# Performance work log

Hardware: AMD Instinct MI355X
Metric: run time of the kernel (lower is better)

The kernel has to match this reference:

```python
import jax, jax.numpy as jnp
import numpy as np

# scNET (vae_flag=False, cd=False, eval mode): genes x cells matrix;
# PPI graph over 3000 genes, KNN graph over 4096 cells.
N_GENES, N_CELLS = 3000, 4096          # col_dim, row_dim
INTER_R, EMBD_R = 512, 128             # gene (rows) encoder dims
INTER_C, EMBD_C = 1024, 256            # cell (cols) encoder dims
N_LAYERS = 2
KNN_E, PPI_E = 65536, 262144
SCALE_PARAM = 3.0                      # TransformerConvReducrLayer scale_param


def setup_inputs() -> dict:
    key = jax.random.key(0)
    ks = iter(jax.random.split(key, 64))
    def lin(shape):
        fan_in = shape[-2]
        return jax.random.normal(next(ks), shape, jnp.float32) / np.sqrt(fan_in)
    inp = {}
    inp["x"] = jax.random.normal(next(ks), (N_GENES, N_CELLS), jnp.float32)
    inp["knn_ei"] = jax.random.randint(next(ks), (2, KNN_E), 0, N_CELLS)
    inp["ppi_ei"] = jax.random.randint(next(ks), (2, PPI_E), 0, N_GENES)
    inp["rl_W"] = lin((N_CELLS, N_CELLS)); inp["rl_b"] = jnp.zeros((N_CELLS,), jnp.float32)
    inp["rs_Wl"] = lin((N_LAYERS, N_CELLS, N_CELLS)); inp["rs_Wr"] = lin((N_LAYERS, N_CELLS, N_CELLS))
    inp["rs_b"] = jnp.zeros((N_LAYERS, N_CELLS), jnp.float32)
    inp["cs_Wl"] = lin((N_LAYERS, N_GENES, N_GENES)); inp["cs_Wr"] = lin((N_LAYERS, N_GENES, N_GENES))
    inp["cs_b"] = jnp.zeros((N_LAYERS, N_GENES), jnp.float32)
    inp["rg_W"] = lin((N_CELLS, INTER_R)); inp["rg_b"] = jnp.zeros((INTER_R,), jnp.float32)
    for nm in ("rq", "rk", "rv", "rsk"):
        inp[nm + "_W"] = lin((INTER_R, EMBD_R)); inp[nm + "_b"] = jnp.zeros((EMBD_R,), jnp.float32)
    inp["cg_W"] = lin((N_GENES, INTER_C)); inp["cg_b"] = jnp.zeros((INTER_C,), jnp.float32)
    for nm in ("cq", "ck", "cv", "csk"):
        inp[nm + "_W"] = lin((INTER_C, EMBD_C)); inp[nm + "_b"] = jnp.zeros((EMBD_C,), jnp.float32)
    inp["d1_W"] = lin((EMBD_C, INTER_C)); inp["d1_b"] = jnp.zeros((INTER_C,), jnp.float32)
    inp["d2_W"] = lin((INTER_C, INTER_C)); inp["d2_b"] = jnp.zeros((INTER_C,), jnp.float32)
    inp["d3_W"] = lin((INTER_C, N_GENES)); inp["d3_b"] = jnp.zeros((N_GENES,), jnp.float32)
    return inp


def sage_conv(x, ei, Wl, Wr, b):
    # PyG SAGEConv (mean aggr, root weight): lin_l(mean_{j->i} x_j) + lin_r(x_i) + b
    n = x.shape[0]
    src, dst = ei[0], ei[1]
    s = jax.ops.segment_sum(x[src], dst, num_segments=n)
    cnt = jax.ops.segment_sum(jnp.ones((ei.shape[1],), x.dtype), dst, num_segments=n)
    agg = s / jnp.maximum(cnt, 1.0)[:, None]
    return agg @ Wl + x @ Wr + b


def gcn_conv(x, ei, W, b):
    # PyG GCNConv: self loops + symmetric D^-1/2 (A+I) D^-1/2 normalization
    n = x.shape[0]
    idx = jnp.arange(n)
    src = jnp.concatenate([ei[0], idx])
    dst = jnp.concatenate([ei[1], idx])
    deg = jax.ops.segment_sum(jnp.ones((src.shape[0],), x.dtype), dst, num_segments=n)
    dinv = jax.lax.rsqrt(jnp.maximum(deg, 1.0))
    h = x @ W
    msg = h[src] * (dinv[src] * dinv[dst])[:, None]
    return jax.ops.segment_sum(msg, dst, num_segments=n) + b


def transformer_conv(x, ei, Wq, bq, Wk, bk, Wv, bv, Ws, bs, scale_param):
    # PyG TransformerConv (heads=1). scale_param=None -> per-destination segment
    # softmax; otherwise scNET's globally sigmoid-normalized attention
    # (TransformerConvReducrLayer.message): global mean/std standardize -> sigmoid.
    n = x.shape[0]
    d = Wq.shape[1]
    src, dst = ei[0], ei[1]
    q = x @ Wq + bq
    k = x @ Wk + bk
    v = x @ Wv + bv
    alpha = (q[dst] * k[src]).sum(-1) / jnp.sqrt(jnp.asarray(d, x.dtype))  # [E]
    if scale_param is None:
        m = jax.ops.segment_max(alpha, dst, num_segments=n)
        e = jnp.exp(alpha - m[dst])
        z = jax.ops.segment_sum(e, dst, num_segments=n)
        alpha = e / (z[dst] + 1e-16)
    else:
        alpha = (alpha - alpha.mean()) / ((1.0 / scale_param) * jnp.std(alpha, ddof=1))
        alpha = jax.nn.sigmoid(alpha)
    out = jax.ops.segment_sum(v[src] * alpha[:, None], dst, num_segments=n)
    return out + (x @ Ws + bs)  # root skip (lin_skip)


def reference(x, knn_ei, ppi_ei, rl_W, rl_b, rs_Wl, rs_Wr, rs_b, cs_Wl, cs_Wr, cs_b,
              rg_W, rg_b, rq_W, rq_b, rk_W, rk_b, rv_W, rv_b, rsk_W, rsk_b,
              cg_W, cg_b, cq_W, cq_b, ck_W, ck_b, cv_W, cv_b, csk_W, csk_b,
              d1_W, d1_b, d2_W, d2_b, d3_W, d3_b):
    # MutaelEncoder: row linear then alternating col/row SAGE layers (dropout=id in eval)
    h = x @ rl_W + rl_b                                   # [G, C]
    for i in range(N_LAYERS):
        h = jax.nn.leaky_relu(sage_conv(h.T, knn_ei, cs_Wl[i], cs_Wr[i], cs_b[i]), 0.01).T
        h = jax.nn.leaky_relu(sage_conv(h, ppi_ei, rs_Wl[i], rs_Wr[i], rs_b[i]), 0.01)
    # rows (gene) DimEncoder: GCN -> LeakyReLU -> TransformerConv (softmax attention)
    r = jax.nn.leaky_relu(gcn_conv(h, ppi_ei, rg_W, rg_b), 0.01)
    row_embed = transformer_conv(r, ppi_ei, rq_W, rq_b, rk_W, rk_b, rv_W, rv_b, rsk_W, rsk_b, None)
    # cols (cell) DimEncoder (reducer): GCN -> LeakyReLU -> sigmoid-normalized attention
    c = jax.nn.leaky_relu(gcn_conv(h.T, knn_ei, cg_W, cg_b), 0.01)
    col_embed = transformer_conv(c, knn_ei, cq_W, cq_b, ck_W, ck_b, cv_W, cv_b, csk_W, csk_b, SCALE_PARAM)
    # FatureDecoder (cd=False): 3-layer MLP with ReLU (dropout=id in eval)
    d = jax.nn.relu(col_embed @ d1_W + d1_b)
    d = jax.nn.relu(d @ d2_W + d2_b)
    recon = d @ d3_W + d3_b                               # [C_cells, G]
    return row_embed, col_embed, recon
```

## Files before the change

kernel.cpp:

```cpp
#include <hip/hip_runtime.h>
#include <math.h>

#define N_GENES 3000
#define N_CELLS 4096
#define GPAD    3072
#define INTER_R 512
#define EMBD_R  128
#define INTER_C 1024
#define EMBD_C  256
#define KNN_E   65536
#define PPI_E   262144

typedef unsigned short u16;
typedef __bf16 bf16x8 __attribute__((ext_vector_type(8)));
typedef float f32x4 __attribute__((ext_vector_type(4)));

__device__ __forceinline__ float b2f(u16 u) {
  union { unsigned i; float f; } x; x.i = ((unsigned)u) << 16; return x.f;
}
__device__ __forceinline__ u16 f2b(float f) {
  union { float f; unsigned i; } x; x.f = f;
  unsigned r = (x.i + 0x7FFFu + ((x.i >> 16) & 1u)) >> 16;
  return (u16)r;
}

typedef const void __attribute__((address_space(1))) gvoid;
typedef void __attribute__((address_space(3))) svoid;
__device__ __forceinline__ void gload16(const void* g, void* l) {
  __builtin_amdgcn_global_load_lds((gvoid*)g, (svoid*)l, 16, 0, 0);
}

template <int OUTF32>
__global__ __launch_bounds__(256) void mgemm_k(
    const u16* __restrict__ A, int lda, const u16* __restrict__ BT, int ldb,
    const float* __restrict__ bias, void* __restrict__ Cv, int ldc,
    int M, int N, int K, int accum, int act, int nbx) {
  __shared__ u16 As[2][64 * 64];
  __shared__ u16 Bs[2][64 * 64];
  const int t = threadIdx.x;
  const int w = t >> 6, l = t & 63;
  const int wr = w >> 1, wc = w & 1;
  const int fr = l & 15, hi = l >> 4;

  int nwg = gridDim.x, bid = blockIdx.x;
  int q = nwg >> 3, r = nwg & 7, xcd = bid & 7, seq = bid >> 3;
  int sid = (xcd < r ? xcd * (q + 1) : r * (q + 1) + (xcd - r) * q) + seq;
  int by = sid / nbx, bx = sid - by * nbx;
  const int row0 = by * 128, col0 = bx * 128;

  f32x4 acc[4][4];
#pragma unroll
  for (int i = 0; i < 4; i++)
#pragma unroll
    for (int j = 0; j < 4; j++) acc[i][j] = (f32x4){0.f, 0.f, 0.f, 0.f};

  const u16* Aad[2]; const u16* Bad[2];
  char* Alds[2]; char* Blds[2];
#pragma unroll
  for (int c = 0; c < 2; c++) {
    int P = (w * 2 + c) * 64 + l;
    int prow = P >> 3, s = P & 7;
    int lr = prow * 2 + (s >> 2);
    int g = (s & 3) ^ (prow & 3);
    int ar = row0 + lr; ar = ar < M ? ar : M - 1;
    int br = col0 + lr; br = br < N ? br : N - 1;
    Aad[c] = A + (size_t)ar * lda + g * 8;
    Bad[c] = BT + (size_t)br * ldb + g * 8;
    Alds[c] = (char*)&As[0][0] + P * 16;
    Blds[c] = (char*)&Bs[0][0] + P * 16;
  }
  const int nt = K >> 5;
  auto stage = [&](int tt, int b) {
    int ko = tt << 5;
#pragma unroll
    for (int c = 0; c < 2; c++) {
      gload16(Aad[c] + ko, Alds[c] + b * 8192);
      gload16(Bad[c] + ko, Blds[c] + b * 8192);
    }
  };
  auto compute = [&](int tt) {
    const u16* Ab = As[tt & 1];
    const u16* Bb = Bs[tt & 1];
    bf16x8 af[4], bfr[4];
#pragma unroll
    for (int mi = 0; mi < 4; mi++) {
      int row = wr * 64 + mi * 16 + fr;
      int pr = row >> 1;
      af[mi] = *(const bf16x8*)&Ab[pr * 64 + ((row & 1) * 4 + (hi ^ (pr & 3))) * 8];
    }
#pragma unroll
    for (int ni = 0; ni < 4; ni++) {
      int row = wc * 64 + ni * 16 + fr;
      int pr = row >> 1;
      bfr[ni] = *(const bf16x8*)&Bb[pr * 64 + ((row & 1) * 4 + (hi ^ (pr & 3))) * 8];
    }
    __builtin_amdgcn_s_setprio(1);
#pragma unroll
    for (int mi = 0; mi < 4; mi++)
#pragma unroll
      for (int ni = 0; ni < 4; ni++)
        acc[mi][ni] = __builtin_amdgcn_mfma_f32_16x16x32_bf16(
            af[mi], bfr[ni], acc[mi][ni], 0, 0, 0);
    __builtin_amdgcn_s_setprio(0);
  };

  stage(0, 0);
  if (nt > 1) stage(1, 1);
  for (int tt = 0; tt < nt - 1; tt++) {
    asm volatile("s_waitcnt vmcnt(4)" ::: "memory");
    __builtin_amdgcn_sched_barrier(0);
    __builtin_amdgcn_s_barrier();
    __builtin_amdgcn_sched_barrier(0);
    compute(tt);
    __builtin_amdgcn_sched_barrier(0);
    __builtin_amdgcn_s_barrier();
    __builtin_amdgcn_sched_barrier(0);
    if (tt + 2 < nt) stage(tt + 2, tt & 1);
  }
  asm volatile("s_waitcnt vmcnt(0)" ::: "memory");
  __builtin_amdgcn_sched_barrier(0);
  __builtin_amdgcn_s_barrier();
  __builtin_amdgcn_sched_barrier(0);
  compute(nt - 1);

#pragma unroll
  for (int mi = 0; mi < 4; mi++) {
    int mb = row0 + wr * 64 + mi * 16 + hi * 4;
#pragma unroll
    for (int rr2 = 0; rr2 < 4; rr2++) {
      int m = mb + rr2;
      if (m >= M) continue;
#pragma unroll
      for (int ni = 0; ni < 4; ni++) {
        int n = col0 + wc * 64 + ni * 16 + fr;
        if (n >= N) continue;
        float v = acc[mi][ni][rr2];
        if (bias) v += bias[n];
        if (OUTF32) {
          float* C = (float*)Cv;
          if (accum) v += C[(size_t)m * ldc + n];
          if (act == 1) v = v > 0.f ? v : 0.01f * v;
          else if (act == 2) v = fmaxf(v, 0.f);
          C[(size_t)m * ldc + n] = v;
        } else {
          u16* C = (u16*)Cv;
          if (accum) v += b2f(C[(size_t)m * ldc + n]);
          if (act == 1) v = v > 0.f ? v : 0.01f * v;
          else if (act == 2) v = fmaxf(v, 0.f);
          C[(size_t)m * ldc + n] = f2b(v);
        }
      }
    }
  }
}

__global__ void cvtw_k(const float* __restrict__ in, int K, int Nw,
                       u16* __restrict__ out, int ldb, int Kpad) {
  __shared__ float tile[32][33];
  int k0 = blockIdx.y * 32, n0 = blockIdx.x * 32;
  int tx = threadIdx.x & 31, ty = threadIdx.x >> 5;
  for (int i = ty; i < 32; i += 8)
    tile[i][tx] = (k0 + i < K && n0 + tx < Nw) ? in[(size_t)(k0 + i) * Nw + n0 + tx] : 0.f;
  __syncthreads();
  for (int i = ty; i < 32; i += 8) {
    int n = n0 + i, k = k0 + tx;
    if (n < Nw && k < Kpad) out[(size_t)n * ldb + k] = f2b(tile[tx][i]);
  }
}

__global__ void tpad_k(const u16* __restrict__ in, int R, int C, int lin,
                       u16* __restrict__ out, int ostride, int Rpad) {
  __shared__ u16 tile[32][33];
  int r0 = blockIdx.y * 32, c0 = blockIdx.x * 32;
  int tx = threadIdx.x & 31, ty = threadIdx.x >> 5;
  for (int i = ty; i < 32; i += 8)
    tile[i][tx] = (r0 + i < R && c0 + tx < C) ? in[(size_t)(r0 + i) * lin + c0 + tx] : (u16)0;
  __syncthreads();
  for (int i = ty; i < 32; i += 8) {
    int c = c0 + i, r = r0 + tx;
    if (c < C && r < Rpad) out[(size_t)c * ostride + r] = tile[tx][i];
  }
}

__global__ void cvtx_k(const float* __restrict__ in, u16* __restrict__ out, int n) {
  int i = (blockIdx.x * 256 + threadIdx.x) * 4;
  if (i >= n) return;
  float4 v = *(const float4*)&in[i];
  uint2 o;
  o.x = (unsigned)f2b(v.x) | ((unsigned)f2b(v.y) << 16);
  o.y = (unsigned)f2b(v.z) | ((unsigned)f2b(v.w) << 16);
  *(uint2*)&out[i] = o;
}

__global__ void catbias_k(const float* b0, const float* b1, const float* b2,
                          const float* b3, int seg, float* out) {
  int i = blockIdx.x * 256 + threadIdx.x;
  if (i >= 4 * seg) return;
  const float* s = i < seg ? b0 : i < 2 * seg ? b1 : i < 3 * seg ? b2 : b3;
  out[i] = s[i & (seg - 1)];
}

__global__ void zero_i32(int* __restrict__ p, int n) {
  int i = blockIdx.x * 256 + threadIdx.x;
  if (i < n) p[i] = 0;
}
__global__ void count_k(const int* __restrict__ dst, int E, int* __restrict__ cnt) {
  int e = blockIdx.x * 256 + threadIdx.x;
  if (e < E) atomicAdd(&cnt[dst[e]], 1);
}
__global__ __launch_bounds__(1024) void scan_k(const int* __restrict__ cnt,
                                               int* __restrict__ rs, int N) {
  __shared__ int sd[1024];
  int t = threadIdx.x;
  int per = (N + 1023) >> 10;
  int base = t * per;
  int loc[4];
  int s = 0;
  for (int u = 0; u < per; u++) {
    int idx = base + u;
    loc[u] = s;
    int v = (idx < N) ? cnt[idx] : 0;
    s += v;
  }
  sd[t] = s;
  __syncthreads();
  for (int off = 1; off < 1024; off <<= 1) {
    int v = (t >= off) ? sd[t - off] : 0;
    __syncthreads();
    sd[t] += v;
    __syncthreads();
  }
  int prev = (t > 0) ? sd[t - 1] : 0;
  for (int u = 0; u < per; u++) {
    int idx = base + u;
    if (idx < N) rs[idx] = prev + loc[u];
  }
  if (t == 0) rs[N] = sd[1023];
}
__global__ void fill_k(const int* __restrict__ src, const int* __restrict__ dst, int E,
                       const int* __restrict__ rs, int* cursor,
                       int* __restrict__ csrc, int* __restrict__ ceid) {
  int e = blockIdx.x * 256 + threadIdx.x;
  if (e >= E) return;
  int d = dst[e];
  int p = atomicAdd(&cursor[d], 1);
  int b = rs[d] + p;
  csrc[b] = src[e];
  ceid[b] = e;
}
__global__ void dinv_k(const int* __restrict__ rs, float* __restrict__ dinv, int N) {
  int i = blockIdx.x * 256 + threadIdx.x;
  if (i < N) dinv[i] = rsqrtf((float)(rs[i + 1] - rs[i] + 1));
}

__global__ void sage_agg_k(const u16* __restrict__ X, int ld, const int* __restrict__ rs,
                           const int* __restrict__ csrc, u16* __restrict__ out, int D) {
  int i = blockIdx.y;
  int j8 = (blockIdx.x * 256 + threadIdx.x) * 8;
  if (j8 >= D) return;
  int s = rs[i], e = rs[i + 1];
  float a[8] = {0, 0, 0, 0, 0, 0, 0, 0};
  for (int p = s; p < e; p++) {
    uint4 v = *(const uint4*)&X[(size_t)csrc[p] * ld + j8];
    a[0] += b2f(v.x & 0xffff); a[1] += b2f(v.x >> 16);
    a[2] += b2f(v.y & 0xffff); a[3] += b2f(v.y >> 16);
    a[4] += b2f(v.z & 0xffff); a[5] += b2f(v.z >> 16);
    a[6] += b2f(v.w & 0xffff); a[7] += b2f(v.w >> 16);
  }
  float inv = 1.f / fmaxf((float)(e - s), 1.f);
  uint4 o;
  o.x = (unsigned)f2b(a[0] * inv) | ((unsigned)f2b(a[1] * inv) << 16);
  o.y = (unsigned)f2b(a[2] * inv) | ((unsigned)f2b(a[3] * inv) << 16);
  o.z = (unsigned)f2b(a[4] * inv) | ((unsigned)f2b(a[5] * inv) << 16);
  o.w = (unsigned)f2b(a[6] * inv) | ((unsigned)f2b(a[7] * inv) << 16);
  *(uint4*)&out[(size_t)i * ld + j8] = o;
}

__global__ void gcn_agg_k(const u16* __restrict__ HW, int ld, const int* __restrict__ rs,
                          const int* __restrict__ csrc, const float* __restrict__ dinv,
                          const float* __restrict__ bias, u16* __restrict__ out, int D) {
  int i = blockIdx.y;
  int j8 = (blockIdx.x * 256 + threadIdx.x) * 8;
  if (j8 >= D) return;
  int s = rs[i], e = rs[i + 1];
  float a[8] = {0, 0, 0, 0, 0, 0, 0, 0};
  for (int p = s; p < e; p++) {
    int sr = csrc[p];
    float w = dinv[sr];
    uint4 v = *(const uint4*)&HW[(size_t)sr * ld + j8];
    a[0] += b2f(v.x & 0xffff) * w; a[1] += b2f(v.x >> 16) * w;
    a[2] += b2f(v.y & 0xffff) * w; a[3] += b2f(v.y >> 16) * w;
    a[4] += b2f(v.z & 0xffff) * w; a[5] += b2f(v.z >> 16) * w;
    a[6] += b2f(v.w & 0xffff) * w; a[7] += b2f(v.w >> 16) * w;
  }
  float di = dinv[i];
  uint4 sv = *(const uint4*)&HW[(size_t)i * ld + j8];
  float sf[8] = {b2f(sv.x & 0xffff), b2f(sv.x >> 16), b2f(sv.y & 0xffff), b2f(sv.y >> 16),
                 b2f(sv.z & 0xffff), b2f(sv.z >> 16), b2f(sv.w & 0xffff), b2f(sv.w >> 16)};
  unsigned o[4];
#pragma unroll
  for (int q = 0; q < 4; q++) {
    float v0 = di * a[2 * q] + sf[2 * q] * di * di + bias[j8 + 2 * q];
    float v1 = di * a[2 * q + 1] + sf[2 * q + 1] * di * di + bias[j8 + 2 * q + 1];
    v0 = v0 > 0.f ? v0 : 0.01f * v0;
    v1 = v1 > 0.f ? v1 : 0.01f * v1;
    o[q] = (unsigned)f2b(v0) | ((unsigned)f2b(v1) << 16);
  }
  *(uint4*)&out[(size_t)i * ld + j8] = *(uint4*)o;
}

__global__ void attn_row_k(const u16* __restrict__ QKVS, const int* __restrict__ rs,
                           const int* __restrict__ csrc, float* __restrict__ out, int N) {
  int node = blockIdx.x * 4 + (threadIdx.x >> 6);
  if (node >= N) return;
  int lane = threadIdx.x & 63;
  const u16* base = QKVS + (size_t)node * 512;
  unsigned qb = *(const unsigned*)&base[lane * 2];
  float qx = b2f(qb & 0xffff), qy = b2f(qb >> 16);
  int s = rs[node], e = rs[node + 1];
  float m = -1e30f, z = 0.f, ax = 0.f, ay = 0.f;
  const float scale = 0.08838834764831845f;
  for (int p = s; p < e; p++) {
    const u16* kb = QKVS + (size_t)csrc[p] * 512;
    unsigned kw = *(const unsigned*)&kb[128 + lane * 2];
    float part = qx * b2f(kw & 0xffff) + qy * b2f(kw >> 16);
#pragma unroll
    for (int off = 32; off; off >>= 1) part += __shfl_xor(part, off);
    float a = part * scale;
    float mn = fmaxf(m, a);
    float sc = __expf(m - mn);
    float wv = __expf(a - mn);
    z = z * sc + wv;
    unsigned vw = *(const unsigned*)&kb[256 + lane * 2];
    ax = ax * sc + wv * b2f(vw & 0xffff);
    ay = ay * sc + wv * b2f(vw >> 16);
    m = mn;
  }
  float inv = (e == s) ? 0.f : 1.f / (z + 1e-16f);
  unsigned sw = *(const unsigned*)&base[384 + lane * 2];
  out[(size_t)node * 128 + lane * 2] = ax * inv + b2f(sw & 0xffff);
  out[(size_t)node * 128 + lane * 2 + 1] = ay * inv + b2f(sw >> 16);
}

__global__ void col_alpha_k(const u16* __restrict__ QKVS, const int* __restrict__ src,
                            const int* __restrict__ dst, float* __restrict__ alpha, int E) {
  int e = blockIdx.x * 4 + (threadIdx.x >> 6);
  if (e >= E) return;
  int lane = threadIdx.x & 63;
  uint2 qb = *(const uint2*)&QKVS[(size_t)dst[e] * 1024 + lane * 4];
  uint2 kb = *(const uint2*)&QKVS[(size_t)src[e] * 1024 + 256 + lane * 4];
  float p = b2f(qb.x & 0xffff) * b2f(kb.x & 0xffff) + b2f(qb.x >> 16) * b2f(kb.x >> 16) +
            b2f(qb.y & 0xffff) * b2f(kb.y & 0xffff) + b2f(qb.y >> 16) * b2f(kb.y >> 16);
#pragma unroll
  for (int off = 32; off; off >>= 1) p += __shfl_xor(p, off);
  if (lane == 0) alpha[e] = p * 0.0625f;
}

__global__ void stats_k(const float* __restrict__ alpha, int E, double* __restrict__ st) {
  __shared__ double s1[256], s2[256];
  int t = threadIdx.x;
  double a1 = 0, a2 = 0;
  for (int i = blockIdx.x * 256 + t; i < E; i += gridDim.x * 256) {
    double a = alpha[i];
    a1 += a; a2 += a * a;
  }
  s1[t] = a1; s2[t] = a2;
  __syncthreads();
  for (int off = 128; off; off >>= 1) {
    if (t < off) { s1[t] += s1[t + off]; s2[t] += s2[t + off]; }
    __syncthreads();
  }
  if (t == 0) { atomicAdd(&st[0], s1[0]); atomicAdd(&st[1], s2[0]); }
}

__global__ void col_attn_agg_k(const u16* __restrict__ QKVS, const float* __restrict__ alpha,
                               const int* __restrict__ rs, const int* __restrict__ csrc,
                               const int* __restrict__ ceid, const double* __restrict__ st,
                               float* __restrict__ outf, u16* __restrict__ outb, int E) {
  int i = blockIdx.x;
  int j = threadIdx.x;
  double mean = st[0] / E;
  double var = (st[1] - E * mean * mean) / (double)(E - 1);
  float rstd = (float)(1.0 / sqrt(var));
  float fm = (float)mean;
  int s = rs[i], e = rs[i + 1];
  float acc = 0.f;
  for (int p = s; p < e; p++) {
    float a = alpha[ceid[p]];
    float x = 3.0f * (a - fm) * rstd;
    float sg = 1.f / (1.f + __expf(-x));
    acc += sg * b2f(QKVS[(size_t)csrc[p] * 1024 + 512 + j]);
  }
  float res = acc + b2f(QKVS[(size_t)i * 1024 + 768 + j]);
  outf[(size_t)i * 256 + j] = res;
  outb[(size_t)i * 256 + j] = f2b(res);
}

extern "C" void kernel_launch(void* const* d_in, const int* in_sizes, int n_in,
                              void* d_out, int out_size, void* d_ws, size_t ws_size,
                              hipStream_t stream) {
  const float* x      = (const float*)d_in[0];
  const int*   knn_ei = (const int*)d_in[1];
  const int*   ppi_ei = (const int*)d_in[2];
  const float* rl_W   = (const float*)d_in[3];
  const float* rl_b   = (const float*)d_in[4];
  const float* rs_Wl  = (const float*)d_in[5];
  const float* rs_Wr  = (const float*)d_in[6];
  const float* rs_b   = (const float*)d_in[7];
  const float* cs_Wl  = (const float*)d_in[8];
  const float* cs_Wr  = (const float*)d_in[9];
  const float* cs_b   = (const float*)d_in[10];
  const float* rg_W   = (const float*)d_in[11];
  const float* rg_b   = (const float*)d_in[12];
  const float* rq_W   = (const float*)d_in[13];
  const float* rq_b   = (const float*)d_in[14];
  const float* rk_W   = (const float*)d_in[15];
  const float* rk_b   = (const float*)d_in[16];
  const float* rv_W   = (const float*)d_in[17];
  const float* rv_b   = (const float*)d_in[18];
  const float* rsk_W  = (const float*)d_in[19];
  const float* rsk_b  = (const float*)d_in[20];
  const float* cg_W   = (const float*)d_in[21];
  const float* cg_b   = (const float*)d_in[22];
  const float* cq_W   = (const float*)d_in[23];
  const float* cq_b   = (const float*)d_in[24];
  const float* ck_W   = (const float*)d_in[25];
  const float* ck_b   = (const float*)d_in[26];
  const float* cv_W   = (const float*)d_in[27];
  const float* cv_b   = (const float*)d_in[28];
  const float* csk_W  = (const float*)d_in[29];
  const float* csk_b  = (const float*)d_in[30];
  const float* d1_W   = (const float*)d_in[31];
  const float* d1_b   = (const float*)d_in[32];
  const float* d2_W   = (const float*)d_in[33];
  const float* d2_b   = (const float*)d_in[34];
  const float* d3_W   = (const float*)d_in[35];
  const float* d3_b   = (const float*)d_in[36];
  float* out = (float*)d_out;

  char* ws = (char*)d_ws;
  size_t off = 0;
  auto alloc = [&](size_t bytes) -> void* {
    void* p = ws + off;
    off = (off + bytes + 255) & ~(size_t)255;
    return p;
  };
  u16* P0 = (u16*)alloc((size_t)N_GENES * N_CELLS * 2);
  u16* P1 = (u16*)alloc((size_t)N_CELLS * GPAD * 2);
  u16* P2 = (u16*)alloc((size_t)N_CELLS * GPAD * 2);
  u16* CR = (u16*)alloc((size_t)N_CELLS * 2 * GPAD * 2);
  u16* BTs = (u16*)alloc((size_t)N_CELLS * 2 * N_CELLS * 2);
  u16* CEb = (u16*)alloc((size_t)N_CELLS * EMBD_C * 2);
  float* catb = (float*)alloc(1024 * 4);
  int* knn_rs  = (int*)alloc((N_CELLS + 1) * 4);
  int* knn_cnt = (int*)alloc(N_CELLS * 4);
  int* knn_cur = (int*)alloc(N_CELLS * 4);
  int* knn_src = (int*)alloc(KNN_E * 4);
  int* knn_eid = (int*)alloc(KNN_E * 4);
  int* ppi_rs  = (int*)alloc((N_GENES + 1) * 4);
  int* ppi_cnt = (int*)alloc(N_GENES * 4);
  int* ppi_cur = (int*)alloc(N_GENES * 4);
  int* ppi_src = (int*)alloc(PPI_E * 4);
  int* ppi_eid = (int*)alloc(PPI_E * 4);
  float* dinv_knn = (float*)alloc(N_CELLS * 4);
  float* dinv_ppi = (float*)alloc(N_GENES * 4);
  float* alphaB   = (float*)alloc(KNN_E * 4);
  double* stats   = (double*)alloc(2 * 8);
  u16* xb = CR;
  u16* CA = CR;
  u16* RA = CR;

  auto cvtw = [&](const float* W, int K, int Nw, u16* dst, int ldb, int Kpad) {
    dim3 g((Nw + 31) / 32, (Kpad + 31) / 32);
    cvtw_k<<<g, 256, 0, stream>>>(W, K, Nw, dst, ldb, Kpad);
  };
  auto mg = [&](const u16* A, int lda, const u16* BT, int ldb, const float* bias,
                void* C, int ldc, int M, int N, int K, int accum, int act, int outf32) {
    int nbx = (N + 127) / 128, nby = (M + 127) / 128;
    dim3 g(nbx * nby);
    if (outf32)
      mgemm_k<1><<<g, 256, 0, stream>>>(A, lda, BT, ldb, bias, C, ldc, M, N, K, accum, act, nbx);
    else
      mgemm_k<0><<<g, 256, 0, stream>>>(A, lda, BT, ldb, bias, C, ldc, M, N, K, accum, act, nbx);
  };
  auto tpad = [&](const u16* in, int R, int C, int lin, u16* o, int ostride, int Rpad) {
    dim3 g((C + 31) / 32, (Rpad + 31) / 32);
    tpad_k<<<g, 256, 0, stream>>>(in, R, C, lin, o, ostride, Rpad);
  };
  auto sage = [&](const u16* X, int ld, const int* rs, const int* csrc, u16* o,
                  int nodes, int D) {
    dim3 g((D / 8 + 255) / 256, nodes);
    sage_agg_k<<<g, 256, 0, stream>>>(X, ld, rs, csrc, o, D);
  };
  auto gcn = [&](const u16* HW, int ld, const int* rs, const int* csrc, const float* dinv,
                 const float* bias, u16* o, int nodes, int D) {
    dim3 g((D / 8 + 255) / 256, nodes);
    gcn_agg_k<<<g, 256, 0, stream>>>(HW, ld, rs, csrc, dinv, bias, o, D);
  };

  zero_i32<<<(N_CELLS + 255) / 256, 256, 0, stream>>>(knn_cnt, N_CELLS);
  count_k<<<(KNN_E + 255) / 256, 256, 0, stream>>>(knn_ei + KNN_E, KNN_E, knn_cnt);
  scan_k<<<1, 1024, 0, stream>>>(knn_cnt, knn_rs, N_CELLS);
  zero_i32<<<(N_CELLS + 255) / 256, 256, 0, stream>>>(knn_cur, N_CELLS);
  fill_k<<<(KNN_E + 255) / 256, 256, 0, stream>>>(knn_ei, knn_ei + KNN_E, KNN_E,
                                                  knn_rs, knn_cur, knn_src, knn_eid);
  dinv_k<<<(N_CELLS + 255) / 256, 256, 0, stream>>>(knn_rs, dinv_knn, N_CELLS);
  zero_i32<<<(N_GENES + 255) / 256, 256, 0, stream>>>(ppi_cnt, N_GENES);
  count_k<<<(PPI_E + 255) / 256, 256, 0, stream>>>(ppi_ei + PPI_E, PPI_E, ppi_cnt);
  scan_k<<<1, 1024, 0, stream>>>(ppi_cnt, ppi_rs, N_GENES);
  zero_i32<<<(N_GENES + 255) / 256, 256, 0, stream>>>(ppi_cur, N_GENES);
  fill_k<<<(PPI_E + 255) / 256, 256, 0, stream>>>(ppi_ei, ppi_ei + PPI_E, PPI_E,
                                                  ppi_rs, ppi_cur, ppi_src, ppi_eid);
  dinv_k<<<(N_GENES + 255) / 256, 256, 0, stream>>>(ppi_rs, dinv_ppi, N_GENES);

  cvtx_k<<<(N_GENES * N_CELLS / 4 + 255) / 256, 256, 0, stream>>>(
      x, xb, N_GENES * N_CELLS);
  cvtw(rl_W, N_CELLS, N_CELLS, BTs, N_CELLS, N_CELLS);
  mg(xb, N_CELLS, BTs, N_CELLS, rl_b, P0, N_CELLS, N_GENES, N_CELLS, N_CELLS, 0, 0, 0);

  for (int i = 0; i < 2; i++) {
    const float* cWl = cs_Wl + (size_t)i * N_GENES * N_GENES;
    const float* cWr = cs_Wr + (size_t)i * N_GENES * N_GENES;
    const float* cb  = cs_b + (size_t)i * N_GENES;
    const float* rWl = rs_Wl + (size_t)i * N_CELLS * N_CELLS;
    const float* rWr = rs_Wr + (size_t)i * N_CELLS * N_CELLS;
    const float* rb  = rs_b + (size_t)i * N_CELLS;
    tpad(P0, N_GENES, N_CELLS, N_CELLS, CA + GPAD, 2 * GPAD, GPAD);
    sage(CA + GPAD, 2 * GPAD, knn_rs, knn_src, CA, N_CELLS, GPAD);
    cvtw(cWl, N_GENES, N_GENES, BTs, 2 * GPAD, GPAD);
    cvtw(cWr, N_GENES, N_GENES, BTs + GPAD, 2 * GPAD, GPAD);
    mg(CA, 2 * GPAD, BTs, 2 * GPAD, cb, P1, GPAD, N_CELLS, N_GENES, 2 * GPAD, 0, 1, 0);
    tpad(P1, N_CELLS, N_GENES, GPAD, RA + N_CELLS, 2 * N_CELLS, N_CELLS);
    sage(RA + N_CELLS, 2 * N_CELLS, ppi_rs, ppi_src, RA, N_GENES, N_CELLS);
    cvtw(rWl, N_CELLS, N_CELLS, BTs, 2 * N_CELLS, N_CELLS);
    cvtw(rWr, N_CELLS, N_CELLS, BTs + N_CELLS, 2 * N_CELLS, N_CELLS);
    mg(RA, 2 * N_CELLS, BTs, 2 * N_CELLS, rb, P0, N_CELLS,
       N_GENES, N_CELLS, 2 * N_CELLS, 0, 1, 0);
  }

  cvtw(rg_W, N_CELLS, INTER_R, BTs, N_CELLS, N_CELLS);
  mg(P0, N_CELLS, BTs, N_CELLS, nullptr, P1, INTER_R, N_GENES, INTER_R, N_CELLS, 0, 0, 0);
  gcn(P1, INTER_R, ppi_rs, ppi_src, dinv_ppi, rg_b, P2, N_GENES, INTER_R);
  cvtw(rq_W, INTER_R, EMBD_R, BTs + (size_t)0 * EMBD_R * INTER_R, INTER_R, INTER_R);
  cvtw(rk_W, INTER_R, EMBD_R, BTs + (size_t)1 * EMBD_R * INTER_R, INTER_R, INTER_R);
  cvtw(rv_W, INTER_R, EMBD_R, BTs + (size_t)2 * EMBD_R * INTER_R, INTER_R, INTER_R);
  cvtw(rsk_W, INTER_R, EMBD_R, BTs + (size_t)3 * EMBD_R * INTER_R, INTER_R, INTER_R);
  catbias_k<<<2, 256, 0, stream>>>(rq_b, rk_b, rv_b, rsk_b, EMBD_R, catb);
  mg(P2, INTER_R, BTs, INTER_R, catb, P1, 4 * EMBD_R, N_GENES, 4 * EMBD_R, INTER_R, 0, 0, 0);
  attn_row_k<<<(N_GENES + 3) / 4, 256, 0, stream>>>(P1, ppi_rs, ppi_src, out, N_GENES);

  tpad(P0, N_GENES, N_CELLS, N_CELLS, P1, GPAD, GPAD);
  cvtw(cg_W, N_GENES, INTER_C, BTs, GPAD, GPAD);
  mg(P1, GPAD, BTs, GPAD, nullptr, P2, INTER_C, N_CELLS, INTER_C, GPAD, 0, 0, 0);
  gcn(P2, INTER_C, knn_rs, knn_src, dinv_knn, cg_b, P0, N_CELLS, INTER_C);
  cvtw(cq_W, INTER_C, EMBD_C, BTs + (size_t)0 * EMBD_C * INTER_C, INTER_C, INTER_C);
  cvtw(ck_W, INTER_C, EMBD_C, BTs + (size_t)1 * EMBD_C * INTER_C, INTER_C, INTER_C);
  cvtw(cv_W, INTER_C, EMBD_C, BTs + (size_t)2 * EMBD_C * INTER_C, INTER_C, INTER_C);
  cvtw(csk_W, INTER_C, EMBD_C, BTs + (size_t)3 * EMBD_C * INTER_C, INTER_C, INTER_C);
  catbias_k<<<4, 256, 0, stream>>>(cq_b, ck_b, cv_b, csk_b, EMBD_C, catb);
  mg(P0, INTER_C, BTs, INTER_C, catb, P1, 4 * EMBD_C, N_CELLS, 4 * EMBD_C, INTER_C, 0, 0, 0);
  col_alpha_k<<<KNN_E / 4, 256, 0, stream>>>(P1, knn_ei, knn_ei + KNN_E, alphaB, KNN_E);
  zero_i32<<<1, 256, 0, stream>>>((int*)stats, 4);
  stats_k<<<64, 256, 0, stream>>>(alphaB, KNN_E, stats);
  float* col_embed = out + (size_t)N_GENES * EMBD_R;
  col_attn_agg_k<<<N_CELLS, 256, 0, stream>>>(P1, alphaB, knn_rs, knn_src, knn_eid,
                                              stats, col_embed, CEb, KNN_E);

  u16* D1 = CR;
  u16* D2 = CR + (size_t)N_CELLS * INTER_C;
  float* recon = col_embed + (size_t)N_CELLS * EMBD_C;
  cvtw(d1_W, EMBD_C, INTER_C, BTs, EMBD_C, EMBD_C);
  mg(CEb, EMBD_C, BTs, EMBD_C, d1_b, D1, INTER_C, N_CELLS, INTER_C, EMBD_C, 0, 2, 0);
  cvtw(d2_W, INTER_C, INTER_C, BTs, INTER_C, INTER_C);
  mg(D1, INTER_C, BTs, INTER_C, d2_b, D2, INTER_C, N_CELLS, INTER_C, INTER_C, 0, 2, 0);
  cvtw(d3_W, INTER_C, N_GENES, BTs, INTER_C, INTER_C);
  mg(D2, INTER_C, BTs, INTER_C, d3_b, recon, N_GENES, N_CELLS, N_GENES, INTER_C, 0, 0, 1);
}
```

Baseline: 2.434 ms.

## Add 256x256 eight-wave pipelined GEMM and slab-wise SAGE aggregation

Adds a new bf16 MFMA GEMM kernel with 256x256 tiles, 512 threads, a swizzled LDS layout, global_load_lds staging and a hand-scheduled double-buffered pipeline. It replaces the old 128x128 GEMM for the large square matmuls and the final decoder layer. The larger tile is meant to raise data reuse per byte loaded and to overlap loads with MFMA work. SAGE aggregation becomes one wave per node, launched once per 512-column slab, which should improve gather locality. The large tiles leave fewer workgroups for the 3000-row problems, and the partial edge tiles waste compute.

New measurement: 2.648 ms. 1.09x slower.

```diff
diff --git a/kernel.cpp b/kernel.cpp
--- a/kernel.cpp
+++ b/kernel.cpp
@@ -28,6 +28,168 @@
 typedef void __attribute__((address_space(3))) svoid;
 __device__ __forceinline__ void gload16(const void* g, void* l) {
   __builtin_amdgcn_global_load_lds((gvoid*)g, (svoid*)l, 16, 0, 0);
+}
+
+template <int OUTF32>
+__global__ __launch_bounds__(512, 1) void mgemm8_k(
+    const u16* __restrict__ A, int lda, const u16* __restrict__ BT, int ldb,
+    const float* __restrict__ bias, void* __restrict__ Cv, int ldc,
+    int M, int N, int K, int accum, int act, int nbx) {
+  __shared__ u16 S[65536];
+  const int t = threadIdx.x;
+  const int wid = t >> 6, l = t & 63;
+  const int wm = wid >> 2, wn = wid & 3;
+  const int fr = l & 15, hi = l >> 4;
+
+  int nwg = gridDim.x, bid = blockIdx.x;
+  int q = nwg >> 3, r = nwg & 7, xcd = bid & 7, seq = bid >> 3;
+  int sid = (xcd < r ? xcd * (q + 1) : r * (q + 1) + (xcd - r) * q) + seq;
+  int by = sid / nbx, bx = sid - by * nbx;
+  const int row0 = by * 256, col0 = bx * 256;
+
+  f32x4 acc[8][4];
+#pragma unroll
+  for (int i = 0; i < 8; i++)
+#pragma unroll
+    for (int j = 0; j < 4; j++) acc[i][j] = (f32x4){0.f, 0.f, 0.f, 0.f};
+
+  int r1 = t >> 2, r2 = r1 + 128;
+  int g1 = (t & 3) ^ ((r1 >> 1) & 3);
+  int g2 = (t & 3) ^ ((r2 >> 1) & 3);
+  int ar1 = row0 + r1; ar1 = ar1 < M ? ar1 : M - 1;
+  int ar2 = row0 + r2; ar2 = ar2 < M ? ar2 : M - 1;
+  int br1 = col0 + r1; br1 = br1 < N ? br1 : N - 1;
+  int br2 = col0 + r2; br2 = br2 < N ? br2 : N - 1;
+  const u16* baseA1 = A + (size_t)ar1 * lda + g1 * 8;
+  const u16* baseA2 = A + (size_t)ar2 * lda + g2 * 8;
+  const u16* baseB1 = BT + (size_t)br1 * ldb + g1 * 8;
+  const u16* baseB2 = BT + (size_t)br2 * ldb + g2 * 8;
+
+  bf16x8 af[4], bfr[4];
+
+#define STAGEA(buf, kh, kt) { \
+  int ko_ = (kt) * 64 + (kh) * 32; \
+  gload16(baseA1 + ko_, (char*)&S[((buf) * 4 + (kh)) * 8192] + t * 16); \
+  gload16(baseA2 + ko_, (char*)&S[((buf) * 4 + (kh)) * 8192] + (t + 512) * 16); }
+#define STAGEB(buf, kh, kt) { \
+  int ko_ = (kt) * 64 + (kh) * 32; \
+  gload16(baseB1 + ko_, (char*)&S[((buf) * 4 + 2 + (kh)) * 8192] + t * 16); \
+  gload16(baseB2 + ko_, (char*)&S[((buf) * 4 + 2 + (kh)) * 8192] + (t + 512) * 16); }
+#define DSRA(buf, kh, mh) \
+  _Pragma("unroll") \
+  for (int i_ = 0; i_ < 4; i_++) { \
+    int row_ = wm * 128 + ((mh) * 4 + i_) * 16 + fr; \
+    af[i_] = *(const bf16x8*)&S[((buf) * 4 + (kh)) * 8192 + row_ * 32 + \
+                                ((hi ^ ((row_ >> 1) & 3)) << 3)]; \
+  }
+#define DSRB(buf, kh) \
+  _Pragma("unroll") \
+  for (int i_ = 0; i_ < 4; i_++) { \
+    int row_ = wn * 64 + i_ * 16 + fr; \
+    bfr[i_] = *(const bf16x8*)&S[((buf) * 4 + 2 + (kh)) * 8192 + row_ * 32 + \
+                                 ((hi ^ ((row_ >> 1) & 3)) << 3)]; \
+  }
+#define MMA(mh) \
+  __builtin_amdgcn_s_setprio(1); \
+  _Pragma("unroll") \
+  for (int i_ = 0; i_ < 4; i_++) { \
+    _Pragma("unroll") \
+    for (int j_ = 0; j_ < 4; j_++) \
+      acc[(mh) * 4 + i_][j_] = __builtin_amdgcn_mfma_f32_16x16x32_bf16( \
+          af[i_], bfr[j_], acc[(mh) * 4 + i_][j_], 0, 0, 0); \
+  } \
+  __builtin_amdgcn_s_setprio(0);
+#define BARMID \
+  __builtin_amdgcn_sched_barrier(0); \
+  __builtin_amdgcn_s_barrier(); \
+  asm volatile("s_waitcnt lgkmcnt(0)" ::: "memory"); \
+  __builtin_amdgcn_sched_barrier(0);
+#define BAREND \
+  __builtin_amdgcn_sched_barrier(0); \
+  __builtin_amdgcn_s_barrier(); \
+  __builtin_amdgcn_sched_barrier(0);
+
+  const int nt = K >> 6;
+  STAGEA(0, 0, 0); STAGEB(0, 0, 0); STAGEA(0, 1, 0); STAGEB(0, 1, 0);
+  STAGEA(1, 0, 1); STAGEB(1, 0, 1); STAGEA(1, 1, 1);
+  asm volatile("s_waitcnt vmcnt(6)" ::: "memory");
+  __builtin_amdgcn_sched_barrier(0);
+  __builtin_amdgcn_s_barrier();
+  __builtin_amdgcn_sched_barrier(0);
+
+  int p = 0;
+  for (int kt = 0; kt < nt - 2; kt++, p ^= 1) {
+    DSRA(p, 0, 0); DSRB(p, 0);
+    STAGEB(p ^ 1, 1, kt + 1);
+    BARMID; MMA(0); BAREND;
+    DSRA(p, 0, 1);
+    STAGEA(p, 0, kt + 2);
+    BARMID; MMA(1); BAREND;
+    DSRA(p, 1, 0); DSRB(p, 1);
+    STAGEB(p, 0, kt + 2);
+    BARMID; MMA(0); BAREND;
+    DSRA(p, 1, 1);
+    STAGEA(p, 1, kt + 2);
+    asm volatile("s_waitcnt vmcnt(6)" ::: "memory");
+    BARMID; MMA(1); BAREND;
+  }
+  DSRA(p, 0, 0); DSRB(p, 0);
+  STAGEB(p ^ 1, 1, nt - 1);
+  BARMID; MMA(0); BAREND;
+  DSRA(p, 0, 1);
+  BARMID; MMA(1); BAREND;
+  DSRA(p, 1, 0); DSRB(p, 1);
+  BARMID; MMA(0); BAREND;
+  DSRA(p, 1, 1);
+  asm volatile("s_waitcnt vmcnt(0)" ::: "memory");
+  BARMID; MMA(1); BAREND;
+  p ^= 1;
+  DSRA(p, 0, 0); DSRB(p, 0);
+  BARMID; MMA(0); BAREND;
+  DSRA(p, 0, 1);
+  BARMID; MMA(1); BAREND;
+  DSRA(p, 1, 0); DSRB(p, 1);
+  BARMID; MMA(0); BAREND;
+  DSRA(p, 1, 1);
+  BARMID; MMA(1); BAREND;
+
+#undef STAGEA
+#undef STAGEB
+#undef DSRA
+#undef DSRB
+#undef MMA
+#undef BARMID
+#undef BAREND
+
+#pragma unroll
+  for (int mf = 0; mf < 8; mf++) {
+    int mb = row0 + wm * 128 + mf * 16 + hi * 4;
+#pragma unroll
+    for (int rr2 = 0; rr2 < 4; rr2++) {
+      int m = mb + rr2;
+      if (m >= M) continue;
+#pragma unroll
+      for (int nf = 0; nf < 4; nf++) {
+        int n = col0 + wn * 64 + nf * 16 + fr;
+        if (n >= N) continue;
+        float v = acc[mf][nf][rr2];
+        if (bias) v += bias[n];
+        if (OUTF32) {
+          float* C = (float*)Cv;
+          if (accum) v += C[(size_t)m * ldc + n];
+          if (act == 1) v = v > 0.f ? v : 0.01f * v;
+          else if (act == 2) v = fmaxf(v, 0.f);
+          C[(size_t)m * ldc + n] = v;
+        } else {
+          u16* C = (u16*)Cv;
+          if (accum) v += b2f(C[(size_t)m * ldc + n]);
+          if (act == 1) v = v > 0.f ? v : 0.01f * v;
+          else if (act == 2) v = fmaxf(v, 0.f);
+          C[(size_t)m * ldc + n] = f2b(v);
+        }
+      }
+    }
+  }
 }
 
 template <int OUTF32>
@@ -253,12 +415,13 @@
   if (i < N) dinv[i] = rsqrtf((float)(rs[i + 1] - rs[i] + 1));
 }
 
-__global__ void sage_agg_k(const u16* __restrict__ X, int ld, const int* __restrict__ rs,
-                           const int* __restrict__ csrc, u16* __restrict__ out, int D) {
-  int i = blockIdx.y;
-  int j8 = (blockIdx.x * 256 + threadIdx.x) * 8;
-  if (j8 >= D) return;
-  int s = rs[i], e = rs[i + 1];
+__global__ void sage_slab_k(const u16* __restrict__ X, int ld, const int* __restrict__ rs,
+                            const int* __restrict__ csrc, u16* __restrict__ out,
+                            int nodes, int Doff) {
+  int node = blockIdx.x * 4 + (threadIdx.x >> 6);
+  if (node >= nodes) return;
+  int j8 = Doff + (threadIdx.x & 63) * 8;
+  int s = rs[node], e = rs[node + 1];
   float a[8] = {0, 0, 0, 0, 0, 0, 0, 0};
   for (int p = s; p < e; p++) {
     uint4 v = *(const uint4*)&X[(size_t)csrc[p] * ld + j8];
@@ -273,7 +436,7 @@
   o.y = (unsigned)f2b(a[2] * inv) | ((unsigned)f2b(a[3] * inv) << 16);
   o.z = (unsigned)f2b(a[4] * inv) | ((unsigned)f2b(a[5] * inv) << 16);
   o.w = (unsigned)f2b(a[6] * inv) | ((unsigned)f2b(a[7] * inv) << 16);
-  *(uint4*)&out[(size_t)i * ld + j8] = o;
+  *(uint4*)&out[(size_t)node * ld + j8] = o;
 }
 
 __global__ void gcn_agg_k(const u16* __restrict__ HW, int ld, const int* __restrict__ rs,
@@ -299,12 +462,12 @@
                  b2f(sv.z & 0xffff), b2f(sv.z >> 16), b2f(sv.w & 0xffff), b2f(sv.w >> 16)};
   unsigned o[4];
 #pragma unroll
-  for (int q = 0; q < 4; q++) {
-    float v0 = di * a[2 * q] + sf[2 * q] * di * di + bias[j8 + 2 * q];
-    float v1 = di * a[2 * q + 1] + sf[2 * q + 1] * di * di + bias[j8 + 2 * q + 1];
+  for (int qq = 0; qq < 4; qq++) {
+    float v0 = di * a[2 * qq] + sf[2 * qq] * di * di + bias[j8 + 2 * qq];
+    float v1 = di * a[2 * qq + 1] + sf[2 * qq + 1] * di * di + bias[j8 + 2 * qq + 1];
     v0 = v0 > 0.f ? v0 : 0.01f * v0;
     v1 = v1 > 0.f ? v1 : 0.01f * v1;
-    o[q] = (unsigned)f2b(v0) | ((unsigned)f2b(v1) << 16);
+    o[qq] = (unsigned)f2b(v0) | ((unsigned)f2b(v1) << 16);
   }
   *(uint4*)&out[(size_t)i * ld + j8] = *(uint4*)o;
 }
@@ -483,14 +646,24 @@
     else
       mgemm_k<0><<<g, 256, 0, stream>>>(A, lda, BT, ldb, bias, C, ldc, M, N, K, accum, act, nbx);
   };
+  auto mg8 = [&](const u16* A, int lda, const u16* BT, int ldb, const float* bias,
+                 void* C, int ldc, int M, int N, int K, int accum, int act, int outf32) {
+    int nbx = (N + 255) / 256, nby = (M + 255) / 256;
+    dim3 g(nbx * nby);
+    if (outf32)
+      mgemm8_k<1><<<g, 512, 0, stream>>>(A, lda, BT, ldb, bias, C, ldc, M, N, K, accum, act, nbx);
+    else
+      mgemm8_k<0><<<g, 512, 0, stream>>>(A, lda, BT, ldb, bias, C, ldc, M, N, K, accum, act, nbx);
+  };
   auto tpad = [&](const u16* in, int R, int C, int lin, u16* o, int ostride, int Rpad) {
     dim3 g((C + 31) / 32, (Rpad + 31) / 32);
     tpad_k<<<g, 256, 0, stream>>>(in, R, C, lin, o, ostride, Rpad);
   };
   auto sage = [&](const u16* X, int ld, const int* rs, const int* csrc, u16* o,
                   int nodes, int D) {
-    dim3 g((D / 8 + 255) / 256, nodes);
-    sage_agg_k<<<g, 256, 0, stream>>>(X, ld, rs, csrc, o, D);
+    int nb = (nodes + 3) / 4;
+    for (int s = 0; s < D; s += 512)
+      sage_slab_k<<<nb, 256, 0, stream>>>(X, ld, rs, csrc, o, nodes, s);
   };
   auto gcn = [&](const u16* HW, int ld, const int* rs, const int* csrc, const float* dinv,
                  const float* bias, u16* o, int nodes, int D) {
@@ -516,7 +689,7 @@
   cvtx_k<<<(N_GENES * N_CELLS / 4 + 255) / 256, 256, 0, stream>>>(
       x, xb, N_GENES * N_CELLS);
   cvtw(rl_W, N_CELLS, N_CELLS, BTs, N_CELLS, N_CELLS);
-  mg(xb, N_CELLS, BTs, N_CELLS, rl_b, P0, N_CELLS, N_GENES, N_CELLS, N_CELLS, 0, 0, 0);
+  mg8(xb, N_CELLS, BTs, N_CELLS, rl_b, P0, N_CELLS, N_GENES, N_CELLS, N_CELLS, 0, 0, 0);
 
   for (int i = 0; i < 2; i++) {
     const float* cWl = cs_Wl + (size_t)i * N_GENES * N_GENES;
@@ -529,13 +702,13 @@
     sage(CA + GPAD, 2 * GPAD, knn_rs, knn_src, CA, N_CELLS, GPAD);
     cvtw(cWl, N_GENES, N_GENES, BTs, 2 * GPAD, GPAD);
     cvtw(cWr, N_GENES, N_GENES, BTs + GPAD, 2 * GPAD, GPAD);
-    mg(CA, 2 * GPAD, BTs, 2 * GPAD, cb, P1, GPAD, N_CELLS, N_GENES, 2 * GPAD, 0, 1, 0);
+    mg8(CA, 2 * GPAD, BTs, 2 * GPAD, cb, P1, GPAD, N_CELLS, N_GENES, 2 * GPAD, 0, 1, 0);
     tpad(P1, N_CELLS, N_GENES, GPAD, RA + N_CELLS, 2 * N_CELLS, N_CELLS);
     sage(RA + N_CELLS, 2 * N_CELLS, ppi_rs, ppi_src, RA, N_GENES, N_CELLS);
     cvtw(rWl, N_CELLS, N_CELLS, BTs, 2 * N_CELLS, N_CELLS);
     cvtw(rWr, N_CELLS, N_CELLS, BTs + N_CELLS, 2 * N_CELLS, N_CELLS);
-    mg(RA, 2 * N_CELLS, BTs, 2 * N_CELLS, rb, P0, N_CELLS,
-       N_GENES, N_CELLS, 2 * N_CELLS, 0, 1, 0);
+    mg8(RA, 2 * N_CELLS, BTs, 2 * N_CELLS, rb, P0, N_CELLS,
+        N_GENES, N_CELLS, 2 * N_CELLS, 0, 1, 0);
   }
 
   cvtw(rg_W, N_CELLS, INTER_R, BTs, N_CELLS, N_CELLS);
@@ -574,5 +747,5 @@
   cvtw(d2_W, INTER_C, INTER_C, BTs, INTER_C, INTER_C);
   mg(D1, INTER_C, BTs, INTER_C, d2_b, D2, INTER_C, N_CELLS, INTER_C, INTER_C, 0, 2, 0);
   cvtw(d3_W, INTER_C, N_GENES, BTs, INTER_C, INTER_C);
-  mg(D2, INTER_C, BTs, INTER_C, d3_b, recon, N_GENES, N_CELLS, N_GENES, INTER_C, 0, 0, 1);
-}
+  mg8(D2, INTER_C, BTs, INTER_C, d3_b, recon, N_GENES, N_CELLS, N_GENES, INTER_C, 0, 0, 1);
+}
```

## Add 192x256 pipelined 8-wave MFMA GEMM and fuse transpose into swapped-operand GEMM

Applied to the files above, without the earlier changes.

Adds a new 512-thread GEMM kernel with 192x256 tiles, a double-buffered LDS pipeline of half-K stages using direct global-to-LDS loads, swizzled LDS reads and MFMA 16x16x32 bf16. The three large GEMMs now use it. The cell-side SAGE GEMM is recomputed as its transpose, swapping operands and applying the bias per row, so it writes straight into the gene-side input layout and the separate transpose kernel is dropped. CA moves to P1 so the buffers do not alias. Larger tiles raise data reuse and the hand-written pipeline overlaps loads with MFMA, at the cost of one workgroup per CU and fewer blocks for the 3000-row shapes.

Result: faster. 2.256 ms (-7.3%).

```diff
diff --git a/kernel.cpp b/kernel.cpp
--- a/kernel.cpp
+++ b/kernel.cpp
@@ -28,6 +28,183 @@
 typedef void __attribute__((address_space(3))) svoid;
 __device__ __forceinline__ void gload16(const void* g, void* l) {
   __builtin_amdgcn_global_load_lds((gvoid*)g, (svoid*)l, 16, 0, 0);
+}
+
+template <int OUTF32, int MF>
+__global__ __launch_bounds__(512, 1) void mgemm8_k(
+    const u16* __restrict__ A, int lda, const u16* __restrict__ BT, int ldb,
+    const float* __restrict__ bias, int biasRow, void* __restrict__ Cv, int ldc,
+    int M, int N, int K, int accum, int act, int nbx) {
+  constexpr int MFH = MF / 2;
+  constexpr int TM = MF * 32;
+  constexpr int ABYTES = TM * 64;
+  constexpr int BBYTES = 16384;
+  constexpr int BUFB = 2 * ABYTES + 2 * BBYTES;
+  __shared__ char S[2 * BUFB];
+  const int t = threadIdx.x;
+  const int wid = t >> 6;
+  const int l = t & 63;
+  const int wm = wid >> 2, wn = wid & 3;
+  const int fr = l & 15, hi = l >> 4;
+
+  int nwg = gridDim.x, bid = blockIdx.x;
+  int q = nwg >> 3, r = nwg & 7, xcd = bid & 7, seq = bid >> 3;
+  int sid = (xcd < r ? xcd * (q + 1) : r * (q + 1) + (xcd - r) * q) + seq;
+  int by = sid / nbx, bx = sid - by * nbx;
+  const int row0 = by * TM, col0 = bx * 256;
+
+  f32x4 acc[MF][4];
+#pragma unroll
+  for (int i = 0; i < MF; i++)
+#pragma unroll
+    for (int j = 0; j < 4; j++) acc[i][j] = (f32x4){0.f, 0.f, 0.f, 0.f};
+
+  const int cA1 = t, cA2 = t + 512;
+  const int rA1 = cA1 >> 2, rA2 = cA2 >> 2;
+  const int gA1 = (cA1 & 3) ^ ((rA1 >> 1) & 3);
+  const int gA2 = (cA2 & 3) ^ ((rA2 >> 1) & 3);
+  int arow1 = row0 + rA1; arow1 = arow1 < M ? arow1 : M - 1;
+  int arow2 = row0 + (rA2 < TM ? rA2 : TM - 1); arow2 = arow2 < M ? arow2 : M - 1;
+  const u16* baseA1 = A + (size_t)arow1 * lda + gA1 * 8;
+  const u16* baseA2 = A + (size_t)arow2 * lda + gA2 * 8;
+  const bool doA2 = (MF == 8) || (t < 256);
+  int brow1 = col0 + rA1; brow1 = brow1 < N ? brow1 : N - 1;
+  int brow2 = col0 + rA2; brow2 = brow2 < N ? brow2 : N - 1;
+  const u16* baseB1 = BT + (size_t)brow1 * ldb + gA1 * 8;
+  const u16* baseB2 = BT + (size_t)brow2 * ldb + gA2 * 8;
+
+  auto aoff = [](int buf, int kh) { return buf * BUFB + kh * ABYTES; };
+  auto boff = [](int buf, int kh) { return buf * BUFB + 2 * ABYTES + kh * BBYTES; };
+
+  auto stageA = [&](int buf, int kh, int kt) {
+    int ko = kt * 64 + kh * 32;
+    gload16(baseA1 + ko, S + aoff(buf, kh) + cA1 * 16);
+    if (doA2) gload16(baseA2 + ko, S + aoff(buf, kh) + cA2 * 16);
+  };
+  auto stageB = [&](int buf, int kh, int kt) {
+    int ko = kt * 64 + kh * 32;
+    gload16(baseB1 + ko, S + boff(buf, kh) + cA1 * 16);
+    gload16(baseB2 + ko, S + boff(buf, kh) + cA2 * 16);
+  };
+
+  bf16x8 af[MFH], bfr[4];
+  auto dsrA = [&](int buf, int kh, int mh) {
+#pragma unroll
+    for (int i = 0; i < MFH; i++) {
+      int row = wm * (MF * 16) + (mh * MFH + i) * 16 + fr;
+      af[i] = *(const bf16x8*)(S + aoff(buf, kh) + row * 64 +
+                               ((hi ^ ((row >> 1) & 3)) << 4));
+    }
+  };
+  auto dsrB = [&](int buf, int kh) {
+#pragma unroll
+    for (int i = 0; i < 4; i++) {
+      int row = wn * 64 + i * 16 + fr;
+      bfr[i] = *(const bf16x8*)(S + boff(buf, kh) + row * 64 +
+                                ((hi ^ ((row >> 1) & 3)) << 4));
+    }
+  };
+  auto mma = [&](int mh) {
+    __builtin_amdgcn_s_setprio(1);
+#pragma unroll
+    for (int i = 0; i < MFH; i++)
+#pragma unroll
+      for (int j = 0; j < 4; j++)
+        acc[mh * MFH + i][j] = __builtin_amdgcn_mfma_f32_16x16x32_bf16(
+            af[i], bfr[j], acc[mh * MFH + i][j], 0, 0, 0);
+    __builtin_amdgcn_s_setprio(0);
+  };
+  auto vmw = [&]() {
+    if (MF == 6 && wid >= 4)
+      asm volatile("s_waitcnt vmcnt(4)" ::: "memory");
+    else
+      asm volatile("s_waitcnt vmcnt(6)" ::: "memory");
+  };
+  auto barmid = [&]() {
+    __builtin_amdgcn_sched_barrier(0);
+    __builtin_amdgcn_s_barrier();
+    asm volatile("s_waitcnt lgkmcnt(0)" ::: "memory");
+    __builtin_amdgcn_sched_barrier(0);
+  };
+  auto barend = [&]() {
+    __builtin_amdgcn_sched_barrier(0);
+    __builtin_amdgcn_s_barrier();
+    __builtin_amdgcn_sched_barrier(0);
+  };
+
+  const int nt = K >> 6;
+  stageA(0, 0, 0); stageB(0, 0, 0); stageA(0, 1, 0); stageB(0, 1, 0);
+  stageA(1, 0, 1); stageB(1, 0, 1); stageA(1, 1, 1);
+  vmw();
+  __builtin_amdgcn_sched_barrier(0);
+  __builtin_amdgcn_s_barrier();
+  __builtin_amdgcn_sched_barrier(0);
+
+  int p = 0;
+  for (int kt = 0; kt < nt - 2; kt++, p ^= 1) {
+    dsrA(p, 0, 0); dsrB(p, 0);
+    stageB(p ^ 1, 1, kt + 1);
+    barmid(); mma(0); barend();
+    dsrA(p, 0, 1);
+    stageA(p, 0, kt + 2);
+    barmid(); mma(1); barend();
+    dsrA(p, 1, 0); dsrB(p, 1);
+    stageB(p, 0, kt + 2);
+    barmid(); mma(0); barend();
+    dsrA(p, 1, 1);
+    stageA(p, 1, kt + 2);
+    vmw();
+    barmid(); mma(1); barend();
+  }
+  dsrA(p, 0, 0); dsrB(p, 0);
+  stageB(p ^ 1, 1, nt - 1);
+  barmid(); mma(0); barend();
+  dsrA(p, 0, 1);
+  barmid(); mma(1); barend();
+  dsrA(p, 1, 0); dsrB(p, 1);
+  barmid(); mma(0); barend();
+  dsrA(p, 1, 1);
+  asm volatile("s_waitcnt vmcnt(0)" ::: "memory");
+  barmid(); mma(1); barend();
+  p ^= 1;
+  dsrA(p, 0, 0); dsrB(p, 0);
+  barmid(); mma(0); barend();
+  dsrA(p, 0, 1);
+  barmid(); mma(1); barend();
+  dsrA(p, 1, 0); dsrB(p, 1);
+  barmid(); mma(0); barend();
+  dsrA(p, 1, 1);
+  barmid(); mma(1); barend();
+
+#pragma unroll
+  for (int mf = 0; mf < MF; mf++) {
+    int mb = row0 + wm * (MF * 16) + mf * 16 + hi * 4;
+#pragma unroll
+    for (int rr2 = 0; rr2 < 4; rr2++) {
+      int m = mb + rr2;
+      if (m >= M) continue;
+#pragma unroll
+      for (int nf = 0; nf < 4; nf++) {
+        int n = col0 + wn * 64 + nf * 16 + fr;
+        if (n >= N) continue;
+        float v = acc[mf][nf][rr2];
+        if (bias) v += biasRow ? bias[m] : bias[n];
+        if (OUTF32) {
+          float* C = (float*)Cv;
+          if (accum) v += C[(size_t)m * ldc + n];
+          if (act == 1) v = v > 0.f ? v : 0.01f * v;
+          else if (act == 2) v = fmaxf(v, 0.f);
+          C[(size_t)m * ldc + n] = v;
+        } else {
+          u16* C = (u16*)Cv;
+          if (accum) v += b2f(C[(size_t)m * ldc + n]);
+          if (act == 1) v = v > 0.f ? v : 0.01f * v;
+          else if (act == 2) v = fmaxf(v, 0.f);
+          C[(size_t)m * ldc + n] = f2b(v);
+        }
+      }
+    }
+  }
 }
 
 template <int OUTF32>
@@ -299,12 +476,12 @@
                  b2f(sv.z & 0xffff), b2f(sv.z >> 16), b2f(sv.w & 0xffff), b2f(sv.w >> 16)};
   unsigned o[4];
 #pragma unroll
-  for (int q = 0; q < 4; q++) {
-    float v0 = di * a[2 * q] + sf[2 * q] * di * di + bias[j8 + 2 * q];
-    float v1 = di * a[2 * q + 1] + sf[2 * q + 1] * di * di + bias[j8 + 2 * q + 1];
+  for (int qq = 0; qq < 4; qq++) {
+    float v0 = di * a[2 * qq] + sf[2 * qq] * di * di + bias[j8 + 2 * qq];
+    float v1 = di * a[2 * qq + 1] + sf[2 * qq + 1] * di * di + bias[j8 + 2 * qq + 1];
     v0 = v0 > 0.f ? v0 : 0.01f * v0;
     v1 = v1 > 0.f ? v1 : 0.01f * v1;
-    o[q] = (unsigned)f2b(v0) | ((unsigned)f2b(v1) << 16);
+    o[qq] = (unsigned)f2b(v0) | ((unsigned)f2b(v1) << 16);
   }
   *(uint4*)&out[(size_t)i * ld + j8] = *(uint4*)o;
 }
@@ -467,8 +644,8 @@
   float* alphaB   = (float*)alloc(KNN_E * 4);
   double* stats   = (double*)alloc(2 * 8);
   u16* xb = CR;
-  u16* CA = CR;
   u16* RA = CR;
+  u16* CA = P1;
 
   auto cvtw = [&](const float* W, int K, int Nw, u16* dst, int ldb, int Kpad) {
     dim3 g((Nw + 31) / 32, (Kpad + 31) / 32);
@@ -482,6 +659,17 @@
       mgemm_k<1><<<g, 256, 0, stream>>>(A, lda, BT, ldb, bias, C, ldc, M, N, K, accum, act, nbx);
     else
       mgemm_k<0><<<g, 256, 0, stream>>>(A, lda, BT, ldb, bias, C, ldc, M, N, K, accum, act, nbx);
+  };
+  auto mg8 = [&](const u16* A, int lda, const u16* BT, int ldb, const float* bias,
+                 int biasRow, void* C, int ldc, int M, int N, int K, int act, int outf32) {
+    int nbx = (N + 255) / 256, nby = (M + 191) / 192;
+    dim3 g(nbx * nby);
+    if (outf32)
+      mgemm8_k<1, 6><<<g, 512, 0, stream>>>(A, lda, BT, ldb, bias, biasRow, C, ldc,
+                                            M, N, K, 0, act, nbx);
+    else
+      mgemm8_k<0, 6><<<g, 512, 0, stream>>>(A, lda, BT, ldb, bias, biasRow, C, ldc,
+                                            M, N, K, 0, act, nbx);
   };
   auto tpad = [&](const u16* in, int R, int C, int lin, u16* o, int ostride, int Rpad) {
     dim3 g((C + 31) / 32, (Rpad + 31) / 32);
@@ -516,7 +704,7 @@
   cvtx_k<<<(N_GENES * N_CELLS / 4 + 255) / 256, 256, 0, stream>>>(
       x, xb, N_GENES * N_CELLS);
   cvtw(rl_W, N_CELLS, N_CELLS, BTs, N_CELLS, N_CELLS);
-  mg(xb, N_CELLS, BTs, N_CELLS, rl_b, P0, N_CELLS, N_GENES, N_CELLS, N_CELLS, 0, 0, 0);
+  mg8(xb, N_CELLS, BTs, N_CELLS, rl_b, 0, P0, N_CELLS, N_GENES, N_CELLS, N_CELLS, 0, 0);
 
   for (int i = 0; i < 2; i++) {
     const float* cWl = cs_Wl + (size_t)i * N_GENES * N_GENES;
@@ -529,13 +717,13 @@
     sage(CA + GPAD, 2 * GPAD, knn_rs, knn_src, CA, N_CELLS, GPAD);
     cvtw(cWl, N_GENES, N_GENES, BTs, 2 * GPAD, GPAD);
     cvtw(cWr, N_GENES, N_GENES, BTs + GPAD, 2 * GPAD, GPAD);
-    mg(CA, 2 * GPAD, BTs, 2 * GPAD, cb, P1, GPAD, N_CELLS, N_GENES, 2 * GPAD, 0, 1, 0);
-    tpad(P1, N_CELLS, N_GENES, GPAD, RA + N_CELLS, 2 * N_CELLS, N_CELLS);
+    mg8(BTs, 2 * GPAD, CA, 2 * GPAD, cb, 1, RA + N_CELLS, 2 * N_CELLS,
+        N_GENES, N_CELLS, 2 * GPAD, 1, 0);
     sage(RA + N_CELLS, 2 * N_CELLS, ppi_rs, ppi_src, RA, N_GENES, N_CELLS);
     cvtw(rWl, N_CELLS, N_CELLS, BTs, 2 * N_CELLS, N_CELLS);
     cvtw(rWr, N_CELLS, N_CELLS, BTs + N_CELLS, 2 * N_CELLS, N_CELLS);
-    mg(RA, 2 * N_CELLS, BTs, 2 * N_CELLS, rb, P0, N_CELLS,
-       N_GENES, N_CELLS, 2 * N_CELLS, 0, 1, 0);
+    mg8(RA, 2 * N_CELLS, BTs, 2 * N_CELLS, rb, 0, P0, N_CELLS,
+        N_GENES, N_CELLS, 2 * N_CELLS, 1, 0);
   }
 
   cvtw(rg_W, N_CELLS, INTER_R, BTs, N_CELLS, N_CELLS);
```
